# Kernel optimization log

Hardware: AMD Instinct MI355X
Metric: run time of the kernel (lower is better)

## Reference

```python
import jax, jax.numpy as jnp
import numpy as np

ALLPASS_DELAYS = [225, 556, 441, 341]
ALLPASS_G = 0.7
COMB_DELAYS = [1116, 1188, 1277, 1356]
COMB_FEEDBACKS = [0.84, 0.82, 0.80, 0.78]


def _lagged_first_order(x, N, g, allpass):
    """Fixed-lag first-order recurrence along axis 0, vectorized over axis 1.

    allpass: y[n] = -g*y[n-N] + x[n] + g*x[n-N]  (n >= N), y[n<N] = 0
    comb:    y[n] =  g*y[n-N] + x[n]             (n >= N), y[n<N] = 0

    The recurrence decouples into N independent stride-N subsequences, so we
    reshape to [blocks, N, W] and lax.scan over blocks (T/N steps instead of T).
    """
    T, W = x.shape
    blocks = -(-T // N)
    Tp = blocks * N
    xb = jnp.pad(x, ((0, Tp - T), (0, 0))).reshape(blocks, N, W)
    zero_blk = jnp.zeros((1, N, W), x.dtype)
    if allpass:
        # drive u[k] = x[k] + g*x[k-1]; block 0 output is forced to zero
        u = jnp.concatenate([zero_blk, xb[1:] + g * xb[:-1]], axis=0)
        a = -g
    else:
        # comb: drive u[k] = x[k] for k>=1; block 0 output is zero
        u = jnp.concatenate([zero_blk, xb[1:]], axis=0)
        a = g

    def step(prev, uk):
        y = uk + a * prev
        return y, y

    _, yb = jax.lax.scan(step, jnp.zeros((N, W), x.dtype), u)
    return yb.reshape(Tp, W)[:T]


def setup_inputs() -> dict:
    key = jax.random.key(0)
    T, W = 131072, 128
    x = jax.random.normal(key, (T, W), dtype=jnp.float32)
    return {"x": x}


def reference(x):
    # Series allpass chain
    for N in ALLPASS_DELAYS:
        x = _lagged_first_order(x, N, ALLPASS_G, allpass=True)
    # Parallel feedback comb bank, summed
    comb = jnp.zeros_like(x)
    for N, g in zip(COMB_DELAYS, COMB_FEEDBACKS):
        comb = comb + _lagged_first_order(x, N, g, allpass=False)
    # Original applies eye(T) @ comb and slices [:, :W]; both are identity ops,
    # so we return comb directly (same math, without materializing a TxT eye).
    return comb
```

## Files before the change

### kernel.cpp

```cpp
#include <hip/hip_runtime.h>


constexpr int W = 128;

template <int V> struct fv { float d[V]; };

template <int V>
__device__ __forceinline__ fv<V> fv_zero() {
  fv<V> r;
#pragma unroll
  for (int c = 0; c < V; ++c) r.d[c] = 0.f;
  return r;
}
using fv2 = fv<2>;
using fv4 = fv<4>;

template <int K, bool PRED>
__device__ __forceinline__
void fmarch_blk(const fv4* __restrict__ x, const fv4* __restrict__ h1,
                const float* __restrict__ pw1, const float* __restrict__ pw2,
                int n0, int N, int laneoff, int Tn, float a,
                fv4& yp, fv4* __restrict__ y) {
  constexpr int RW = W / 4;
  fv4 xs[K], t1[K], t2[K];
  float p1[K], p2[K];
#pragma unroll
  for (int u = 0; u < K; ++u) {
    const int n = n0 + u * N;
    const bool ok = !PRED || n < Tn;
    const int q1 = n / 225, r1 = n - q1 * 225;
    const int q2 = n / 556, r2 = n - q2 * 556;
    xs[u] = ok ? x[n * RW + laneoff] : fv_zero<4>();
    t1[u] = x[r1 * RW + laneoff];
    t2[u] = h1[r2 * RW + laneoff];
    p1[u] = ok ? pw1[q1] : 0.f;
    p2[u] = ok ? pw2[q2] : 0.f;
  }
#pragma unroll
  for (int u = 0; u < K; ++u) {
#pragma unroll
    for (int c = 0; c < 4; ++c) {
      float s = fmaf(-p1[u], t1[u].d[c], xs[u].d[c]);
      s = fmaf(-p2[u], t2[u].d[c], s);
      yp.d[c] = fmaf(a, yp.d[c], s);
    }
    y[u] = yp;
  }
}

template <int CNT, bool PRED, int U>
__device__ __forceinline__
void fmarch_seg(const fv4* __restrict__ x, const fv4* __restrict__ h1,
                const float* __restrict__ pw1, const float* __restrict__ pw2,
                int n0, int N, int laneoff, int Tn, float a,
                fv4& yp, fv4* __restrict__ y) {
  constexpr int NB = CNT / U, R = CNT % U;
#pragma unroll
  for (int b = 0; b < NB; ++b)
    fmarch_blk<U, PRED>(x, h1, pw1, pw2, n0 + b * U * N, N, laneoff, Tn, a,
                        yp, y + b * U);
  if constexpr (R > 0)
    fmarch_blk<R, PRED>(x, h1, pw1, pw2, n0 + NB * U * N, N, laneoff, Tn, a,
                        yp, y + NB * U);
}

template <int MODE, int K, bool PRED>
__device__ __forceinline__
void fstore_blk(fv4* __restrict__ out, int n0, int N, int laneoff, int Tn,
                float a, fv4 Yin, const fv4* __restrict__ y, float& p) {
  constexpr int RW = W / 4;
  fv4 os[K];
  if constexpr (MODE == 2) {
#pragma unroll
    for (int u = 0; u < K; ++u) {
      const int n = n0 + u * N;
      os[u] = (!PRED || n < Tn) ? out[n * RW + laneoff] : fv_zero<4>();
    }
  }
#pragma unroll
  for (int u = 0; u < K; ++u) {
    const int n = n0 + u * N;
    fv4 v;
#pragma unroll
    for (int c = 0; c < 4; ++c) {
      v.d[c] = fmaf(p, Yin.d[c], y[u].d[c]);
      if constexpr (MODE == 2) v.d[c] += os[u].d[c];
    }
    if (!PRED || n < Tn) out[n * RW + laneoff] = v;
    p *= a;
  }
}

template <int MODE, int CNT, bool PRED, int U>
__device__ __forceinline__
void fstore_seg(fv4* __restrict__ out, int n0, int N, int laneoff, int Tn,
                float a, fv4 Yin, const fv4* __restrict__ y, float p0) {
  constexpr int NB = CNT / U, R = CNT % U;
  float p = p0;
#pragma unroll
  for (int b = 0; b < NB; ++b)
    fstore_blk<MODE, U, PRED>(out, n0 + b * U * N, N, laneoff, Tn, a, Yin,
                              y + b * U, p);
  if constexpr (R > 0)
    fstore_blk<MODE, R, PRED>(out, n0 + NB * U * N, N, laneoff, Tn, a, Yin,
                              y + NB * U, p);
}

template <int MODE, int S, int L, bool ODDN, int UM, int US>
__global__ __launch_bounds__(S * 64, 2)
void fcomb(const fv4* __restrict__ x, const fv4* __restrict__ h1,
           const float* __restrict__ pw1, const float* __restrict__ pw2,
           fv4* __restrict__ out, int N, float g, float aL, int T, int items) {
  const float a = g;
  __shared__ fv4 C[S][64];
  const int tid = threadIdx.x;
  const int s  = tid >> 6;
  const int l6 = tid & 63;
  const int laneoff = l6 & 31;

  for (int item = blockIdx.x; item < items; item += gridDim.x) {
    const int r  = (item << 1) | (l6 >> 5);
    const int Tn = (!ODDN || r < N) ? T : 0;
    const int n0 = s * L * N + r;

    fv4 y[L];
    fv4 yp = fv_zero<4>();

    if (s == 0) {
      y[0] = fv_zero<4>();
      fmarch_seg<L - 1, ODDN, UM>(x, h1, pw1, pw2, n0 + N, N, laneoff, Tn, a,
                                  yp, y + 1);
    } else if (!ODDN && s < S - 1) {
      fmarch_seg<L, false, UM>(x, h1, pw1, pw2, n0, N, laneoff, Tn, a, yp, y);
    } else {
      fmarch_seg<L, true, UM>(x, h1, pw1, pw2, n0, N, laneoff, Tn, a, yp, y);
    }
    C[s][l6] = yp;
    __syncthreads();

    fv4 Yin = fv_zero<4>();
    for (int j = 0; j < s; ++j) {
#pragma unroll
      for (int c = 0; c < 4; ++c)
        Yin.d[c] = fmaf(aL, Yin.d[c], C[j][l6].d[c]);
    }
    __syncthreads();

    if (!ODDN && s < S - 1)
      fstore_seg<MODE, L, false, US>(out, n0, N, laneoff, Tn, a, Yin, y, a);
    else
      fstore_seg<MODE, L, true, US>(out, n0, N, laneoff, Tn, a, Yin, y, a);
  }
}

__global__ void prep_pw(float* __restrict__ pw1, float* __restrict__ pw2) {
  if (threadIdx.x == 0) {
    float p = 1.f;
    for (int m = 0; m < 1024; ++m) { pw1[m] = p; p *= -0.7f; }
  } else if (threadIdx.x == 64) {
    float p = 1.f;
    for (int m = 0; m < 512; ++m) { pw2[m] = p; p *= -0.7f; }
  }
}

__global__ __launch_bounds__(256)
void prep_h1(const fv2* __restrict__ x, fv2* __restrict__ h1) {
  const int e = blockIdx.x * 256 + threadIdx.x;
  if (e >= 556 * 64) return;
  const int n = e >> 6;
  fv2 v;
  if (n < 225) {
    v = fv_zero<2>();
  } else {
    v = x[e];
    const int   d = (n < 450) ? 225 : 450;
    const float c = (n < 450) ? 0.7f : -0.49f;
    fv2 t = x[e - d * 64];
    v.d[0] = fmaf(c, t.d[0], v.d[0]);
    v.d[1] = fmaf(c, t.d[1], v.d[1]);
  }
  h1[e] = v;
}

constexpr int W2 = 64;
template <int MODE, bool STORE>
__device__ __forceinline__
void g_march(const float2* __restrict__ in, float2* __restrict__ out,
             int n, int N, int cnt, int T, int lane, float g, float a,
             float2& xp, float2& yp) {
  for (int j = 0; j < cnt; ++j) {
    float2 x = (n < T) ? in[n * W2 + lane] : make_float2(0.f, 0.f);
    float ux = (MODE == 0) ? fmaf(g, xp.x, x.x) : x.x;
    float uy = (MODE == 0) ? fmaf(g, xp.y, x.y) : x.y;
    yp.x = fmaf(a, yp.x, ux);
    yp.y = fmaf(a, yp.y, uy);
    xp = x;
    if (STORE && n < T) {
      float2 v = yp;
      if (MODE == 2) { v.x += out[n * W2 + lane].x; v.y += out[n * W2 + lane].y; }
      out[n * W2 + lane] = v;
    }
    n += N;
  }
}

template <int MODE>
__global__ __launch_bounds__(1024)
void stage_gen(const float2* __restrict__ in, float2* __restrict__ out,
               int N, float g, float aL, int L, int T) {
  const float a = (MODE == 0) ? -g : g;
  __shared__ float2 C[16][W2];
  const int tid = threadIdx.x, s = tid >> 6, lane = tid & 63;
  const int r = blockIdx.x;
  if (r >= T) return;
  const int n0 = s * L * N + r;
  if (s == 0) {
    float2 xp = make_float2(0.f, 0.f), yp = make_float2(0.f, 0.f);
    if (MODE == 0) xp = in[r * W2 + lane];
    if (MODE != 2) out[r * W2 + lane] = make_float2(0.f, 0.f);
    g_march<MODE, true>(in, out, r + N, N, L - 1, T, lane, g, a, xp, yp);
    C[0][lane] = yp;
    __syncthreads();
    return;
  }
  {
    float2 xp = make_float2(0.f, 0.f), yp = make_float2(0.f, 0.f);
    if (MODE == 0) xp = in[(n0 - N) * W2 + lane];
    g_march<MODE, false>(in, out, n0, N, L, T, lane, g, a, xp, yp);
    C[s][lane] = yp;
  }
  __syncthreads();
  float2 Yin = make_float2(0.f, 0.f);
  for (int j = 0; j < s; ++j) {
    Yin.x = fmaf(aL, Yin.x, C[j][lane].x);
    Yin.y = fmaf(aL, Yin.y, C[j][lane].y);
  }
  float2 xp = make_float2(0.f, 0.f), yp = Yin;
  if (MODE == 0) xp = in[(n0 - N) * W2 + lane];
  g_march<MODE, true>(in, out, n0, N, L, T, lane, g, a, xp, yp);
}

static void pick_SL(int T, int N, int S0, int* Sp, int* Lp) {
  int Kmin = T / N, Kmax = (T + N - 1) / N;
  int S = S0;
  for (; S > 1; --S) {
    int L = (Kmax + S - 1) / S;
    if ((S - 1) * L <= Kmin) break;
  }
  *Sp = S;
  *Lp = (Kmax + *Sp - 1) / *Sp;
}

static float pow_f(float a, int n) {
  double p = 1.0;
  for (int i = 0; i < n; ++i) p *= (double)a;
  return (float)p;
}

extern "C" void kernel_launch(void* const* d_in, const int* in_sizes, int n_in,
                              void* d_out, int out_size, void* d_ws, size_t ws_size,
                              hipStream_t stream) {
  float* out = (float*)d_out;
  float* ws  = (float*)d_ws;
  const float* x = (const float*)d_in[0];
  const int T = in_sizes[0] / W;

  if (T == 131072) {
    float* h1f = ws;
    float* pw1 = ws + 556 * 128;
    float* pw2 = pw1 + 1024;

    hipLaunchKernelGGL(prep_pw, dim3(1), dim3(128), 0, stream, pw1, pw2);
    hipLaunchKernelGGL(prep_h1, dim3(139), dim3(256), 0, stream,
                       (const fv2*)x, (fv2*)h1f);

    const fv4* x4  = (const fv4*)x;
    const fv4* h14 = (const fv4*)h1f;
    fv4* o4 = (fv4*)out;

    hipLaunchKernelGGL((fcomb<1, 8, 15, false, 2, 4>), dim3(512), dim3(512),
                       0, stream, x4, h14, pw1, pw2, o4,
                       1116, 0.84f, pow_f(0.84f, 15), T, 558);
    hipLaunchKernelGGL((fcomb<2, 8, 14, false, 2, 4>), dim3(512), dim3(512),
                       0, stream, x4, h14, pw1, pw2, o4,
                       1188, 0.82f, pow_f(0.82f, 14), T, 594);
    hipLaunchKernelGGL((fcomb<2, 8, 13, true, 2, 4>), dim3(512), dim3(512),
                       0, stream, x4, h14, pw1, pw2, o4,
                       1277, 0.80f, pow_f(0.80f, 13), T, 639);
    hipLaunchKernelGGL((fcomb<2, 8, 13, false, 2, 4>), dim3(512), dim3(512),
                       0, stream, x4, h14, pw1, pw2, o4,
                       1356, 0.78f, pow_f(0.78f, 13), T, 678);
  } else {
    const int   apN[4] = {225, 556, 441, 341};
    const int   cbN[4] = {1116, 1188, 1277, 1356};
    const float cbG[4] = {0.84f, 0.82f, 0.80f, 0.78f};
    const float2* src = (const float2*)x;
    float2* bufs[2] = {(float2*)out, (float2*)ws};
    int cur = 0;
    for (int i = 0; i < 4; ++i) {
      int S, L;
      pick_SL(T, apN[i], 16, &S, &L);
      hipLaunchKernelGGL((stage_gen<0>), dim3(apN[i]), dim3(S * 64), 0, stream,
                         src, bufs[cur], apN[i], 0.7f, pow_f(-0.7f, L), L, T);
      src = bufs[cur];
      cur ^= 1;
    }
    float2* dst = (src == (float2*)out) ? (float2*)ws : (float2*)out;
    for (int i = 0; i < 4; ++i) {
      int S, L;
      pick_SL(T, cbN[i], 16, &S, &L);
      if (i == 0)
        hipLaunchKernelGGL((stage_gen<1>), dim3(cbN[i]), dim3(S * 64), 0, stream,
                           src, dst, cbN[i], cbG[i], pow_f(cbG[i], L), L, T);
      else
        hipLaunchKernelGGL((stage_gen<2>), dim3(cbN[i]), dim3(S * 64), 0, stream,
                           src, dst, cbN[i], cbG[i], pow_f(cbG[i], L), L, T);
    }
    if (dst != (float2*)out)
      hipMemcpyAsync(out, dst, (size_t)T * W * sizeof(float),
                     hipMemcpyDeviceToDevice, stream);
  }
}
```

Measured before the change: 277.1 us.

## Precompute allpass-filtered signal once and feed it to all comb kernels

Adds a prep_s kernel that evaluates the closed-form allpass chain (x minus power-weighted terms from x and h1) once per sample and writes it to workspace. The four comb kernels then stream this single buffer instead of each recomputing the gathers, integer divisions and FMAs. h1 and the power tables are moved into the output buffer as scratch, and the march unroll goes from 2 to 4. In exchange it adds one full T×W write and read pass and relies on the first comb kernel overwriting the scratch region in out only after prep_s has consumed it.

```diff
diff --git a/kernel.cpp b/kernel.cpp
--- a/kernel.cpp
+++ b/kernel.cpp
@@ -17,51 +17,34 @@
 
 template <int K, bool PRED>
 __device__ __forceinline__
-void fmarch_blk(const fv4* __restrict__ x, const fv4* __restrict__ h1,
-                const float* __restrict__ pw1, const float* __restrict__ pw2,
-                int n0, int N, int laneoff, int Tn, float a,
-                fv4& yp, fv4* __restrict__ y) {
+void fmarch_blk(const fv4* __restrict__ sb, int n0, int N, int laneoff,
+                int Tn, float a, fv4& yp, fv4* __restrict__ y) {
   constexpr int RW = W / 4;
-  fv4 xs[K], t1[K], t2[K];
-  float p1[K], p2[K];
+  fv4 xs[K];
 #pragma unroll
   for (int u = 0; u < K; ++u) {
     const int n = n0 + u * N;
-    const bool ok = !PRED || n < Tn;
-    const int q1 = n / 225, r1 = n - q1 * 225;
-    const int q2 = n / 556, r2 = n - q2 * 556;
-    xs[u] = ok ? x[n * RW + laneoff] : fv_zero<4>();
-    t1[u] = x[r1 * RW + laneoff];
-    t2[u] = h1[r2 * RW + laneoff];
-    p1[u] = ok ? pw1[q1] : 0.f;
-    p2[u] = ok ? pw2[q2] : 0.f;
+    xs[u] = (!PRED || n < Tn) ? sb[n * RW + laneoff] : fv_zero<4>();
   }
 #pragma unroll
   for (int u = 0; u < K; ++u) {
 #pragma unroll
-    for (int c = 0; c < 4; ++c) {
-      float s = fmaf(-p1[u], t1[u].d[c], xs[u].d[c]);
-      s = fmaf(-p2[u], t2[u].d[c], s);
-      yp.d[c] = fmaf(a, yp.d[c], s);
-    }
+    for (int c = 0; c < 4; ++c)
+      yp.d[c] = fmaf(a, yp.d[c], xs[u].d[c]);
     y[u] = yp;
   }
 }
 
 template <int CNT, bool PRED, int U>
 __device__ __forceinline__
-void fmarch_seg(const fv4* __restrict__ x, const fv4* __restrict__ h1,
-                const float* __restrict__ pw1, const float* __restrict__ pw2,
-                int n0, int N, int laneoff, int Tn, float a,
-                fv4& yp, fv4* __restrict__ y) {
+void fmarch_seg(const fv4* __restrict__ sb, int n0, int N, int laneoff,
+                int Tn, float a, fv4& yp, fv4* __restrict__ y) {
   constexpr int NB = CNT / U, R = CNT % U;
 #pragma unroll
   for (int b = 0; b < NB; ++b)
-    fmarch_blk<U, PRED>(x, h1, pw1, pw2, n0 + b * U * N, N, laneoff, Tn, a,
-                        yp, y + b * U);
+    fmarch_blk<U, PRED>(sb, n0 + b * U * N, N, laneoff, Tn, a, yp, y + b * U);
   if constexpr (R > 0)
-    fmarch_blk<R, PRED>(x, h1, pw1, pw2, n0 + NB * U * N, N, laneoff, Tn, a,
-                        yp, y + NB * U);
+    fmarch_blk<R, PRED>(sb, n0 + NB * U * N, N, laneoff, Tn, a, yp, y + NB * U);
 }
 
 template <int MODE, int K, bool PRED>
@@ -108,9 +91,8 @@
 
 template <int MODE, int S, int L, bool ODDN, int UM, int US>
 __global__ __launch_bounds__(S * 64, 2)
-void fcomb(const fv4* __restrict__ x, const fv4* __restrict__ h1,
-           const float* __restrict__ pw1, const float* __restrict__ pw2,
-           fv4* __restrict__ out, int N, float g, float aL, int T, int items) {
+void fcomb(const fv4* __restrict__ sb, fv4* __restrict__ out,
+           int N, float g, float aL, int T, int items) {
   const float a = g;
   __shared__ fv4 C[S][64];
   const int tid = threadIdx.x;
@@ -128,12 +110,11 @@
 
     if (s == 0) {
       y[0] = fv_zero<4>();
-      fmarch_seg<L - 1, ODDN, UM>(x, h1, pw1, pw2, n0 + N, N, laneoff, Tn, a,
-                                  yp, y + 1);
+      fmarch_seg<L - 1, ODDN, UM>(sb, n0 + N, N, laneoff, Tn, a, yp, y + 1);
     } else if (!ODDN && s < S - 1) {
-      fmarch_seg<L, false, UM>(x, h1, pw1, pw2, n0, N, laneoff, Tn, a, yp, y);
+      fmarch_seg<L, false, UM>(sb, n0, N, laneoff, Tn, a, yp, y);
     } else {
-      fmarch_seg<L, true, UM>(x, h1, pw1, pw2, n0, N, laneoff, Tn, a, yp, y);
+      fmarch_seg<L, true, UM>(sb, n0, N, laneoff, Tn, a, yp, y);
     }
     C[s][l6] = yp;
     __syncthreads();
@@ -180,6 +161,29 @@
     v.d[1] = fmaf(c, t.d[1], v.d[1]);
   }
   h1[e] = v;
+}
+
+__global__ __launch_bounds__(1024)
+void prep_s(const fv4* __restrict__ x, const fv4* __restrict__ h1,
+            const float* __restrict__ pw1, const float* __restrict__ pw2,
+            fv4* __restrict__ sb) {
+  const int e = blockIdx.x * 1024 + threadIdx.x;
+  const int n  = e >> 5;
+  const int lo = e & 31;
+  const int q1 = n / 225, r1 = n - q1 * 225;
+  const int q2 = n / 556, r2 = n - q2 * 556;
+  const fv4 xs = x[e];
+  const fv4 t1 = x[r1 * 32 + lo];
+  const fv4 t2 = h1[r2 * 32 + lo];
+  const float p1 = pw1[q1];
+  const float p2 = pw2[q2];
+  fv4 v;
+#pragma unroll
+  for (int c = 0; c < 4; ++c) {
+    float s = fmaf(-p1, t1.d[c], xs.d[c]);
+    v.d[c] = fmaf(-p2, t2.d[c], s);
+  }
+  sb[e] = v;
 }
 
 constexpr int W2 = 64;
@@ -266,30 +270,28 @@
   const int T = in_sizes[0] / W;
 
   if (T == 131072) {
-    float* h1f = ws;
-    float* pw1 = ws + 556 * 128;
+    float* h1f = out;
+    float* pw1 = out + 556 * 128;
     float* pw2 = pw1 + 1024;
+    float* sbf = ws;
 
     hipLaunchKernelGGL(prep_pw, dim3(1), dim3(128), 0, stream, pw1, pw2);
     hipLaunchKernelGGL(prep_h1, dim3(139), dim3(256), 0, stream,
                        (const fv2*)x, (fv2*)h1f);
-
-    const fv4* x4  = (const fv4*)x;
-    const fv4* h14 = (const fv4*)h1f;
+    hipLaunchKernelGGL(prep_s, dim3(4096), dim3(1024), 0, stream,
+                       (const fv4*)x, (const fv4*)h1f, pw1, pw2, (fv4*)sbf);
+
+    const fv4* s4 = (const fv4*)sbf;
     fv4* o4 = (fv4*)out;
 
-    hipLaunchKernelGGL((fcomb<1, 8, 15, false, 2, 4>), dim3(512), dim3(512),
-                       0, stream, x4, h14, pw1, pw2, o4,
-                       1116, 0.84f, pow_f(0.84f, 15), T, 558);
-    hipLaunchKernelGGL((fcomb<2, 8, 14, false, 2, 4>), dim3(512), dim3(512),
-                       0, stream, x4, h14, pw1, pw2, o4,
-                       1188, 0.82f, pow_f(0.82f, 14), T, 594);
-    hipLaunchKernelGGL((fcomb<2, 8, 13, true, 2, 4>), dim3(512), dim3(512),
-                       0, stream, x4, h14, pw1, pw2, o4,
-                       1277, 0.80f, pow_f(0.80f, 13), T, 639);
-    hipLaunchKernelGGL((fcomb<2, 8, 13, false, 2, 4>), dim3(512), dim3(512),
-                       0, stream, x4, h14, pw1, pw2, o4,
-                       1356, 0.78f, pow_f(0.78f, 13), T, 678);
+    hipLaunchKernelGGL((fcomb<1, 8, 15, false, 4, 4>), dim3(512), dim3(512),
+                       0, stream, s4, o4, 1116, 0.84f, pow_f(0.84f, 15), T, 558);
+    hipLaunchKernelGGL((fcomb<2, 8, 14, false, 4, 4>), dim3(512), dim3(512),
+                       0, stream, s4, o4, 1188, 0.82f, pow_f(0.82f, 14), T, 594);
+    hipLaunchKernelGGL((fcomb<2, 8, 13, true, 4, 4>), dim3(512), dim3(512),
+                       0, stream, s4, o4, 1277, 0.80f, pow_f(0.80f, 13), T, 639);
+    hipLaunchKernelGGL((fcomb<2, 8, 13, false, 4, 4>), dim3(512), dim3(512),
+                       0, stream, s4, o4, 1356, 0.78f, pow_f(0.78f, 13), T, 678);
   } else {
     const int   apN[4] = {225, 556, 441, 341};
     const int   cbN[4] = {1116, 1188, 1277, 1356};
```

Result: faster. 255.2 us (-7.9%).
